# Optimization experiments

Hardware: AMD Instinct MI355X
Metric: run time of the kernel (lower is better)

Reference implementation:

```python
import jax, jax.numpy as jnp
import numpy as np

N, E, D, H, G = 50000, 800000, 256, 256, 64
EPS = 1e-5

def setup_inputs() -> dict:
    key = jax.random.key(0)
    ks = jax.random.split(key, 16)
    s_in = float(np.sqrt(2.0 / D))   # He fan_in init
    s_h = float(np.sqrt(2.0 / H))
    inp = {}
    inp['x'] = jax.random.normal(ks[0], (N, D), jnp.float32)
    inp['edge_index'] = jax.random.randint(ks[1], (2, E), 0, N)
    inp['batch'] = jnp.sort(jax.random.randint(ks[2], (N,), 0, G))
    inp['bn_in_g'] = jnp.ones((D,), jnp.float32)
    inp['bn_in_b'] = jnp.zeros((D,), jnp.float32)
    for i in range(3):
        fan = D if i == 0 else H
        inp[f'W{i}'] = jax.random.normal(ks[3 + i], (fan, H), jnp.float32) * float(np.sqrt(2.0 / fan))
        inp[f'b{i}'] = jnp.zeros((H,), jnp.float32)
        inp[f'bn{i}_g'] = jnp.ones((H,), jnp.float32)
        inp[f'bn{i}_b'] = jnp.zeros((H,), jnp.float32)
    inp['Wa1'] = jax.random.normal(ks[6], (H, H // 2), jnp.float32) * s_h
    inp['ba1'] = jnp.zeros((H // 2,), jnp.float32)
    inp['Wa2'] = jax.random.normal(ks[7], (H // 2, 1), jnp.float32) * float(np.sqrt(2.0 / (H // 2)))
    inp['ba2'] = jnp.zeros((1,), jnp.float32)
    inp['Wo'] = jax.random.normal(ks[8], (H, 2), jnp.float32) * s_h
    inp['bo'] = jnp.zeros((2,), jnp.float32)
    return inp


def _bn(x, g, b):
    # BatchNorm1d, batch statistics (training-mode normalization), biased var
    m = jnp.mean(x, axis=0)
    v = jnp.mean(jnp.square(x - m), axis=0)
    return (x - m) * jax.lax.rsqrt(v + EPS) * g + b


def _gcn(x, src, dst, W, b):
    h = x @ W  # [N, H]
    n = x.shape[0]
    deg = jax.ops.segment_sum(jnp.ones_like(src, x.dtype), dst, num_segments=n) + 1.0  # +1 self-loop
    dinv = jax.lax.rsqrt(deg)  # [N]
    msg = h[src] * (dinv[src] * dinv[dst])[:, None]          # gather + edgewise scale
    agg = jax.ops.segment_sum(msg, dst, num_segments=n)      # scatter-add at dst
    return agg + h * (dinv * dinv)[:, None] + b               # self-loop term fused


def reference(x, edge_index, batch, bn_in_g, bn_in_b,
              W0, b0, bn0_g, bn0_b, W1, b1, bn1_g, bn1_b, W2, b2, bn2_g, bn2_b,
              Wa1, ba1, Wa2, ba2, Wo, bo):
    src, dst = edge_index[0], edge_index[1]
    x = _bn(x, bn_in_g, bn_in_b)  # dropout = identity (eval)
    # layer 0
    xp = _bn(jax.nn.relu(_gcn(x, src, dst, W0, b0)), bn0_g, bn0_b)
    # layers 1..2 with residual
    for (W, b, g, bb) in ((W1, b1, bn1_g, bn1_b), (W2, b2, bn2_g, bn2_b)):
        xn = _bn(jax.nn.relu(_gcn(xp, src, dst, W, b)), g, bb)
        xp = xn + xp
    # attention over all nodes (softmax along node dim, as in source)
    scores = jax.nn.leaky_relu(xp @ Wa1 + ba1, 0.01) @ Wa2 + ba2  # [N,1]
    w = jax.nn.softmax(scores, axis=0)
    xw = xp * w
    cnt = jax.ops.segment_sum(jnp.ones((xp.shape[0],), xp.dtype), batch, num_segments=G)
    pooled = jax.ops.segment_sum(xw, batch, num_segments=G) / jnp.maximum(cnt, 1.0)[:, None]
    return pooled @ Wo + bo  # [G, 2]
```

## Files before the change

### kernel.cpp

```cpp
#include <hip/hip_runtime.h>

#define N_NODES 50000
#define N_EDGES 800000
#define DIM 256
#define NG 64
#define EPS_BN 1e-5f
#define NB_AGG 3125
#define NB_COL 512

typedef _Float16 f16;
typedef _Float16 half8 __attribute__((ext_vector_type(8)));
typedef _Float16 half4 __attribute__((ext_vector_type(4)));
typedef float floatx4 __attribute__((ext_vector_type(4)));

__global__ __launch_bounds__(256) void col_stats_kernel(const float* __restrict__ X, int n,
                                                        float* __restrict__ part) {
    int c = threadIdx.x;
    float s = 0.f, q = 0.f;
    for (int i = blockIdx.x; i < n; i += gridDim.x) {
        float v = X[(size_t)i * DIM + c];
        s += v; q += v * v;
    }
    part[(size_t)c * NB_COL + blockIdx.x] = s;
    part[(size_t)(DIM + c) * NB_COL + blockIdx.x] = q;
}

__global__ __launch_bounds__(256) void reduce_stats_kernel(const float* __restrict__ part, int nrows,
                                                           float* __restrict__ stats) {
    int wave = threadIdx.x >> 6, lane = threadIdx.x & 63;
    int c = blockIdx.x * 4 + wave;
    float t = 0.f;
    for (int i = lane; i < nrows; i += 64) t += part[(size_t)c * nrows + i];
    for (int o = 32; o > 0; o >>= 1) t += __shfl_down(t, o);
    if (lane == 0) stats[c] = t;
}

__global__ void finalize_stats_kernel(const float* __restrict__ sums, float* __restrict__ mr, float inv_n) {
    int c = threadIdx.x;
    float m = sums[c] * inv_n;
    float v = sums[DIM + c] * inv_n - m * m;
    mr[c] = m;
    mr[DIM + c] = rsqrtf(v + EPS_BN);
}

__global__ __launch_bounds__(256) void bn_apply_in_kernel(const float* __restrict__ Xin, f16* __restrict__ Af,
                                                          const float* __restrict__ mr, const float* __restrict__ g,
                                                          const float* __restrict__ b, int n) {
    int c = threadIdx.x;
    float mean = mr[c], rstd = mr[DIM + c], gg = g[c], bb = b[c];
    for (int i = blockIdx.x; i < n; i += gridDim.x) {
        size_t idx = (size_t)i * DIM + c;
        float v = Xin[idx];
        v = (v - mean) * rstd * gg + bb;
        Af[idx] = (f16)v;
    }
}

__global__ __launch_bounds__(256) void bn_apply_kernel(const f16* __restrict__ Cin, f16* __restrict__ Af,
                                                       const float* __restrict__ mr, const float* __restrict__ g,
                                                       const float* __restrict__ b, int n, int residual) {
    int c = threadIdx.x;
    float mean = mr[c], rstd = mr[DIM + c], gg = g[c], bb = b[c];
    for (int i = blockIdx.x; i < n; i += gridDim.x) {
        size_t idx = (size_t)i * DIM + c;
        float v = (float)Cin[idx];
        v = fmaxf(v, 0.f);
        v = (v - mean) * rstd * gg + bb;
        if (residual) v += (float)Af[idx];
        Af[idx] = (f16)v;
    }
}

__global__ void convert_wT_kernel(const float* __restrict__ W, f16* __restrict__ Wt, int K, int M) {
    int idx = blockIdx.x * 256 + threadIdx.x;
    if (idx < K * M) {
        int m = idx / K, k = idx % K;
        Wt[idx] = (f16)W[(size_t)k * M + m];
    }
}

__global__ void count_int_kernel(const int* __restrict__ idx, int n, int* __restrict__ cnt) {
    for (int i = blockIdx.x * blockDim.x + threadIdx.x; i < n; i += gridDim.x * blockDim.x)
        atomicAdd(&cnt[idx[i]], 1);
}

#define SCHUNK 2048
__global__ __launch_bounds__(256) void scan1_kernel(const int* __restrict__ cnt, int n,
                                                    int* __restrict__ outp, int* __restrict__ bsums,
                                                    float* __restrict__ dinv) {
    __shared__ int lds[256];
    int t = threadIdx.x;
    int base = blockIdx.x * SCHUNK + t * 8;
    int v[8]; int s = 0;
#pragma unroll
    for (int j = 0; j < 8; j++) {
        int id = base + j;
        int x = 0;
        if (id < n) { x = cnt[id]; dinv[id] = rsqrtf((float)x + 1.0f); }
        v[j] = s; s += x;
    }
    lds[t] = s; __syncthreads();
    for (int o = 1; o < 256; o <<= 1) {
        int add = (t >= o) ? lds[t - o] : 0;
        __syncthreads();
        lds[t] += add;
        __syncthreads();
    }
    int excl = lds[t] - s;
#pragma unroll
    for (int j = 0; j < 8; j++) { int id = base + j; if (id < n) outp[id] = excl + v[j]; }
    if (t == 255) bsums[blockIdx.x] = lds[255];
}

__global__ void scan2_kernel(int* bsums, int nb) {
    if (threadIdx.x == 0 && blockIdx.x == 0) {
        int r = 0;
        for (int i = 0; i < nb; i++) { int t = bsums[i]; bsums[i] = r; r += t; }
    }
}

__global__ void scan3_kernel(int* __restrict__ outp, const int* __restrict__ bsums, int n, int total) {
    int i = blockIdx.x * blockDim.x + threadIdx.x;
    if (i < n) outp[i] += bsums[i / SCHUNK];
    if (i == 0) outp[n] = total;
}

__global__ void scatter_kernel(const int* __restrict__ src, const int* __restrict__ dst, int ne,
                               const int* __restrict__ rowp, int* __restrict__ fill, int* __restrict__ ss) {
    for (int e = blockIdx.x * blockDim.x + threadIdx.x; e < ne; e += gridDim.x * blockDim.x) {
        int d = dst[e];
        int pos = rowp[d] + atomicAdd(&fill[d], 1);
        ss[pos] = src[e];
    }
}

__global__ void graph_bounds_kernel(const int* __restrict__ batch, int n, int* __restrict__ start) {
    int i = blockIdx.x * blockDim.x + threadIdx.x;
    if (i < n) {
        int b = batch[i];
        if (i == 0 || batch[i - 1] != b) start[b] = i;
    }
}

__global__ void graph_offsets2_kernel(const int* __restrict__ start, int* __restrict__ off, int* __restrict__ cnt) {
    if (threadIdx.x == 0 && blockIdx.x == 0) {
        int nxt = N_NODES;
        for (int g = NG - 1; g >= 0; --g) {
            int s = start[g];
            int o = (s < 0) ? nxt : s;
            off[g] = o;
            cnt[g] = nxt - o;
            nxt = o;
        }
    }
}

__global__ __launch_bounds__(256) void gcn_agg_kernel(const f16* __restrict__ h, const int* __restrict__ rowp,
                                                      const int* __restrict__ ss, const float* __restrict__ dinv,
                                                      const float* __restrict__ bias, f16* __restrict__ out,
                                                      float* __restrict__ part, int n) {
    int wave = threadIdx.x >> 6;
    int lane = threadIdx.x & 63;
    int c = lane * 4;
    float4 bv = *(const float4*)&bias[c];
    float s0 = 0.f, s1 = 0.f, s2 = 0.f, s3 = 0.f;
    float q0 = 0.f, q1 = 0.f, q2 = 0.f, q3 = 0.f;
    for (int row = blockIdx.x * 4 + wave; row < n; row += gridDim.x * 4) {
        float ax = 0.f, ay = 0.f, az = 0.f, aw = 0.f;
        int e0 = rowp[row], e1 = rowp[row + 1];
        int e = e0;
        for (; e + 3 < e1; e += 4) {
            int i0 = ss[e], i1 = ss[e + 1], i2 = ss[e + 2], i3 = ss[e + 3];
            float w0 = dinv[i0], w1 = dinv[i1], w2 = dinv[i2], w3 = dinv[i3];
            half4 h0 = *(const half4*)&h[(size_t)i0 * DIM + c];
            half4 h1 = *(const half4*)&h[(size_t)i1 * DIM + c];
            half4 h2 = *(const half4*)&h[(size_t)i2 * DIM + c];
            half4 h3 = *(const half4*)&h[(size_t)i3 * DIM + c];
            ax += w0 * (float)h0[0] + w1 * (float)h1[0] + w2 * (float)h2[0] + w3 * (float)h3[0];
            ay += w0 * (float)h0[1] + w1 * (float)h1[1] + w2 * (float)h2[1] + w3 * (float)h3[1];
            az += w0 * (float)h0[2] + w1 * (float)h1[2] + w2 * (float)h2[2] + w3 * (float)h3[2];
            aw += w0 * (float)h0[3] + w1 * (float)h1[3] + w2 * (float)h2[3] + w3 * (float)h3[3];
        }
        for (; e < e1; e++) {
            int si = ss[e];
            float ww = dinv[si];
            half4 hv = *(const half4*)&h[(size_t)si * DIM + c];
            ax += ww * (float)hv[0]; ay += ww * (float)hv[1];
            az += ww * (float)hv[2]; aw += ww * (float)hv[3];
        }
        float di = dinv[row];
        float d2 = di * di;
        half4 hs = *(const half4*)&h[(size_t)row * DIM + c];
        float rx = di * ax + d2 * (float)hs[0] + bv.x;
        float ry = di * ay + d2 * (float)hs[1] + bv.y;
        float rz = di * az + d2 * (float)hs[2] + bv.z;
        float rw = di * aw + d2 * (float)hs[3] + bv.w;
        half4 o; o[0] = (f16)rx; o[1] = (f16)ry; o[2] = (f16)rz; o[3] = (f16)rw;
        *(half4*)&out[(size_t)row * DIM + c] = o;
        float t;
        t = fmaxf(rx, 0.f); s0 += t; q0 += t * t;
        t = fmaxf(ry, 0.f); s1 += t; q1 += t * t;
        t = fmaxf(rz, 0.f); s2 += t; q2 += t * t;
        t = fmaxf(rw, 0.f); s3 += t; q3 += t * t;
    }
    __shared__ float sred[4][64][4];
    __shared__ float qred[4][64][4];
    sred[wave][lane][0] = s0; sred[wave][lane][1] = s1; sred[wave][lane][2] = s2; sred[wave][lane][3] = s3;
    qred[wave][lane][0] = q0; qred[wave][lane][1] = q1; qred[wave][lane][2] = q2; qred[wave][lane][3] = q3;
    __syncthreads();
    if (wave == 0) {
        int b = blockIdx.x;
#pragma unroll
        for (int j = 0; j < 4; j++) {
            float a = 0.f, qq = 0.f;
#pragma unroll
            for (int ww = 0; ww < 4; ww++) { a += sred[ww][lane][j]; qq += qred[ww][lane][j]; }
            part[(size_t)(c + j) * NB_AGG + b] = a;
            part[(size_t)(DIM + c + j) * NB_AGG + b] = qq;
        }
    }
}

#define BM 128
#define BN 128
#define BK 32
#define LDP 40
__global__ __launch_bounds__(256) void gemm_f16_kernel(const f16* __restrict__ Af, const f16* __restrict__ Wt,
                                                       f16* __restrict__ C, int n, int K, int M) {
    __shared__ __align__(16) f16 As[BM * LDP];
    __shared__ __align__(16) f16 Bs[BN * LDP];
    int tid = threadIdx.x;
    int wave = tid >> 6, lane = tid & 63;
    int wm = wave >> 1, wn = wave & 1;
    int q = lane >> 4, l16 = lane & 15;
    int bm = blockIdx.x * BM, bn = blockIdx.y * BN;
    floatx4 acc[4][4] = {};
    for (int k0 = 0; k0 < K; k0 += BK) {
#pragma unroll
        for (int rr = 0; rr < 2; rr++) {
            int cidx = tid + rr * 256;
            int row = cidx >> 2, off = (cidx & 3) * 8;
            int arow = bm + row; if (arow >= n) arow = n - 1;
            *(float4*)&As[row * LDP + off] = *(const float4*)&Af[(size_t)arow * K + k0 + off];
            int brow = bn + row;
            *(float4*)&Bs[row * LDP + off] = *(const float4*)&Wt[(size_t)brow * K + k0 + off];
        }
        __syncthreads();
        half8 af[4], bf[4];
#pragma unroll
        for (int i = 0; i < 4; i++) af[i] = *(half8*)&As[(wm * 64 + i * 16 + l16) * LDP + q * 8];
#pragma unroll
        for (int j = 0; j < 4; j++) bf[j] = *(half8*)&Bs[(wn * 64 + j * 16 + l16) * LDP + q * 8];
#pragma unroll
        for (int i = 0; i < 4; i++)
#pragma unroll
            for (int j = 0; j < 4; j++)
                acc[i][j] = __builtin_amdgcn_mfma_f32_16x16x32_f16(af[i], bf[j], acc[i][j], 0, 0, 0);
        __syncthreads();
    }
#pragma unroll
    for (int i = 0; i < 4; i++)
#pragma unroll
        for (int j = 0; j < 4; j++) {
            int col = bn + wn * 64 + j * 16 + l16;
#pragma unroll
            for (int r = 0; r < 4; r++) {
                int row = bm + wm * 64 + i * 16 + q * 4 + r;
                if (row < n) C[(size_t)row * M + col] = (f16)acc[i][j][r];
            }
        }
}

__global__ __launch_bounds__(256) void gemm_attn_kernel(const f16* __restrict__ Af, const f16* __restrict__ Wt,
                                                        const float* __restrict__ ba1, const float* __restrict__ Wa2,
                                                        const float* __restrict__ ba2, float* __restrict__ score,
                                                        int n, int K) {
    __shared__ __align__(16) f16 As[BM * LDP];
    __shared__ __align__(16) f16 Bs[128 * LDP];
    __shared__ float scred[128][2];
    int tid = threadIdx.x;
    int wave = tid >> 6, lane = tid & 63;
    int wm = wave >> 1, wn = wave & 1;
    int q = lane >> 4, l16 = lane & 15;
    int bm = blockIdx.x * BM;
    floatx4 acc[4][4] = {};
    for (int k0 = 0; k0 < K; k0 += BK) {
#pragma unroll
        for (int rr = 0; rr < 2; rr++) {
            int cidx = tid + rr * 256;
            int row = cidx >> 2, off = (cidx & 3) * 8;
            int arow = bm + row; if (arow >= n) arow = n - 1;
            *(float4*)&As[row * LDP + off] = *(const float4*)&Af[(size_t)arow * K + k0 + off];
            *(float4*)&Bs[row * LDP + off] = *(const float4*)&Wt[(size_t)row * K + k0 + off];
        }
        __syncthreads();
        half8 af[4], bf[4];
#pragma unroll
        for (int i = 0; i < 4; i++) af[i] = *(half8*)&As[(wm * 64 + i * 16 + l16) * LDP + q * 8];
#pragma unroll
        for (int j = 0; j < 4; j++) bf[j] = *(half8*)&Bs[(wn * 64 + j * 16 + l16) * LDP + q * 8];
#pragma unroll
        for (int i = 0; i < 4; i++)
#pragma unroll
            for (int j = 0; j < 4; j++)
                acc[i][j] = __builtin_amdgcn_mfma_f32_16x16x32_f16(af[i], bf[j], acc[i][j], 0, 0, 0);
        __syncthreads();
    }
    float ba1v[4], wa2v[4];
#pragma unroll
    for (int j = 0; j < 4; j++) {
        int col = wn * 64 + j * 16 + l16;
        ba1v[j] = ba1[col];
        wa2v[j] = Wa2[col];
    }
#pragma unroll
    for (int i = 0; i < 4; i++)
#pragma unroll
        for (int r = 0; r < 4; r++) {
            float p = 0.f;
#pragma unroll
            for (int j = 0; j < 4; j++) {
                float v = acc[i][j][r] + ba1v[j];
                v = (v > 0.f) ? v : 0.01f * v;
                p += v * wa2v[j];
            }
#pragma unroll
            for (int o = 1; o < 16; o <<= 1) p += __shfl_xor(p, o);
            if (l16 == 0) scred[wm * 64 + i * 16 + q * 4 + r][wn] = p;
        }
    __syncthreads();
    if (tid < 128) {
        int grow = bm + tid;
        if (grow < n) score[grow] = scred[tid][0] + scred[tid][1] + ba2[0];
    }
}

__global__ __launch_bounds__(256) void reduce_max_kernel(const float* __restrict__ s, int n, float* __restrict__ part) {
    __shared__ float lds[256];
    float m = -3.0e38f;
    for (int i = blockIdx.x * 256 + threadIdx.x; i < n; i += gridDim.x * 256) m = fmaxf(m, s[i]);
    lds[threadIdx.x] = m; __syncthreads();
    for (int o = 128; o > 0; o >>= 1) {
        if (threadIdx.x < o) lds[threadIdx.x] = fmaxf(lds[threadIdx.x], lds[threadIdx.x + o]);
        __syncthreads();
    }
    if (threadIdx.x == 0) part[blockIdx.x] = lds[0];
}

__global__ __launch_bounds__(256) void reduce_sumexp_kernel(const float* __restrict__ s, int n,
                                                            const float* __restrict__ part_max,
                                                            float* __restrict__ part_sum) {
    __shared__ float lds[256];
    int t = threadIdx.x;
    lds[t] = part_max[t]; __syncthreads();
    for (int o = 128; o > 0; o >>= 1) {
        if (t < o) lds[t] = fmaxf(lds[t], lds[t + o]);
        __syncthreads();
    }
    float mx = lds[0];
    __syncthreads();
    float acc = 0.f;
    for (int i = blockIdx.x * 256 + t; i < n; i += gridDim.x * 256) acc += expf(s[i] - mx);
    lds[t] = acc; __syncthreads();
    for (int o = 128; o > 0; o >>= 1) {
        if (t < o) lds[t] += lds[t + o];
        __syncthreads();
    }
    if (t == 0) part_sum[blockIdx.x] = lds[0];
}

__global__ __launch_bounds__(256) void pool_kernel(const f16* __restrict__ Af, const float* __restrict__ score,
                                                   const int* __restrict__ offs, const int* __restrict__ cnts,
                                                   const float* __restrict__ part_max, float* __restrict__ pooled) {
    __shared__ float lds[256];
    int c = threadIdx.x;
    lds[c] = part_max[c]; __syncthreads();
    for (int o = 128; o > 0; o >>= 1) {
        if (c < o) lds[c] = fmaxf(lds[c], lds[c + o]);
        __syncthreads();
    }
    float mx = lds[0];
    int g = blockIdx.x;
    int st = offs[g], cn = cnts[g];
    float acc = 0.f;
    for (int i = (int)blockIdx.y; i < cn; i += 32) {
        int i1 = i + 8, i2 = i + 16, i3 = i + 24;
        float s0 = score[st + i];
        float s1 = (i1 < cn) ? score[st + i1] : -3.0e38f;
        float s2 = (i2 < cn) ? score[st + i2] : -3.0e38f;
        float s3 = (i3 < cn) ? score[st + i3] : -3.0e38f;
        float a0 = (float)Af[(size_t)(st + i) * DIM + c];
        float a1 = (i1 < cn) ? (float)Af[(size_t)(st + i1) * DIM + c] : 0.f;
        float a2 = (i2 < cn) ? (float)Af[(size_t)(st + i2) * DIM + c] : 0.f;
        float a3 = (i3 < cn) ? (float)Af[(size_t)(st + i3) * DIM + c] : 0.f;
        acc += a0 * expf(s0 - mx) + a1 * expf(s1 - mx) + a2 * expf(s2 - mx) + a3 * expf(s3 - mx);
    }
    atomicAdd(&pooled[g * DIM + c], acc);
}

__global__ __launch_bounds__(256) void out_kernel(const float* __restrict__ pooled, const int* __restrict__ cnt,
                                                  const float* __restrict__ part_sum, const float* __restrict__ Wo,
                                                  const float* __restrict__ bo, float* __restrict__ out) {
    __shared__ float l0[256], l1[256];
    int g = blockIdx.x, c = threadIdx.x;
    l0[c] = part_sum[c]; __syncthreads();
    for (int o = 128; o > 0; o >>= 1) {
        if (c < o) l0[c] += l0[c + o];
        __syncthreads();
    }
    float denom = l0[0];
    __syncthreads();
    float scale = 1.f / (denom * fmaxf((float)cnt[g], 1.f));
    float v = pooled[g * DIM + c] * scale;
    l0[c] = v * Wo[c * 2];
    l1[c] = v * Wo[c * 2 + 1];
    __syncthreads();
    for (int o = 128; o > 0; o >>= 1) {
        if (c < o) { l0[c] += l0[c + o]; l1[c] += l1[c + o]; }
        __syncthreads();
    }
    if (c == 0) { out[g * 2] = l0[0] + bo[0]; out[g * 2 + 1] = l1[0] + bo[1]; }
}

extern "C" void kernel_launch(void* const* d_in, const int* in_sizes, int n_in,
                              void* d_out, int out_size, void* d_ws, size_t ws_size,
                              hipStream_t stream) {
    const float* x       = (const float*)d_in[0];
    const int*   ei      = (const int*)d_in[1];
    const int*   batch   = (const int*)d_in[2];
    const float* bn_in_g = (const float*)d_in[3];
    const float* bn_in_b = (const float*)d_in[4];
    const float* Ws[3]   = {(const float*)d_in[5],  (const float*)d_in[9],  (const float*)d_in[13]};
    const float* bs[3]   = {(const float*)d_in[6],  (const float*)d_in[10], (const float*)d_in[14]};
    const float* gs[3]   = {(const float*)d_in[7],  (const float*)d_in[11], (const float*)d_in[15]};
    const float* bbs[3]  = {(const float*)d_in[8],  (const float*)d_in[12], (const float*)d_in[16]};
    const float* Wa1 = (const float*)d_in[17];
    const float* ba1 = (const float*)d_in[18];
    const float* Wa2 = (const float*)d_in[19];
    const float* ba2 = (const float*)d_in[20];
    const float* Wo  = (const float*)d_in[21];
    const float* bo  = (const float*)d_in[22];

    char* w = (char*)d_ws;
    size_t off = 0;
    auto alloc = [&](size_t bytes) -> void* {
        void* p = w + off;
        off += (bytes + 255) & ~(size_t)255;
        return p;
    };
    int*   deg     = (int*)alloc((size_t)N_NODES * 4);
    int*   fill    = (int*)alloc((size_t)N_NODES * 4);
    float* pooled  = (float*)alloc((size_t)NG * DIM * 4);
    size_t zero_span = off;
    float* stats_part = (float*)alloc((size_t)512 * NB_AGG * 4);
    float* statsS  = (float*)alloc(512 * 4);
    f16*   Afh  = (f16*)alloc((size_t)N_NODES * DIM * 2);
    f16*   Bh   = (f16*)alloc((size_t)N_NODES * DIM * 2);
    f16*   Ch   = (f16*)alloc((size_t)N_NODES * DIM * 2);
    f16*   Wt[3];
    for (int l = 0; l < 3; l++) Wt[l] = (f16*)alloc((size_t)DIM * DIM * 2);
    f16*   Wa1t = (f16*)alloc((size_t)128 * DIM * 2);
    int* sorted_src = (int*)alloc((size_t)N_EDGES * 4);
    float* dinv = (float*)alloc((size_t)N_NODES * 4);
    int* rowp   = (int*)alloc((size_t)(N_NODES + 1) * 4);
    float* score = (float*)alloc((size_t)N_NODES * 4);
    float* mr    = (float*)alloc(512 * 4);
    int* bsums   = (int*)alloc(64 * 4);
    float* part_max = (float*)alloc(256 * 4);
    float* part_sum = (float*)alloc(256 * 4);
    int* gstart  = (int*)alloc(64 * 4);
    int* cnt_g   = (int*)alloc(64 * 4);
    int* off_g   = (int*)alloc(64 * 4);

    const int* src = ei;
    const int* dst = ei + N_EDGES;
    const int NSCAN = (N_NODES + SCHUNK - 1) / SCHUNK;

    hipMemsetAsync(d_ws, 0, zero_span, stream);
    hipMemsetAsync(gstart, 0xff, 64 * 4, stream);

    count_int_kernel<<<3125, 256, 0, stream>>>(dst, N_EDGES, deg);
    scan1_kernel<<<NSCAN, 256, 0, stream>>>(deg, N_NODES, rowp, bsums, dinv);
    scan2_kernel<<<1, 64, 0, stream>>>(bsums, NSCAN);
    scan3_kernel<<<(N_NODES + 255) / 256, 256, 0, stream>>>(rowp, bsums, N_NODES, N_EDGES);
    scatter_kernel<<<3125, 256, 0, stream>>>(src, dst, N_EDGES, rowp, fill, sorted_src);

    graph_bounds_kernel<<<(N_NODES + 255) / 256, 256, 0, stream>>>(batch, N_NODES, gstart);
    graph_offsets2_kernel<<<1, 64, 0, stream>>>(gstart, off_g, cnt_g);

    for (int l = 0; l < 3; l++)
        convert_wT_kernel<<<DIM * DIM / 256, 256, 0, stream>>>(Ws[l], Wt[l], DIM, DIM);
    convert_wT_kernel<<<128 * DIM / 256, 256, 0, stream>>>(Wa1, Wa1t, DIM, 128);

    col_stats_kernel<<<NB_COL, 256, 0, stream>>>(x, N_NODES, stats_part);
    reduce_stats_kernel<<<128, 256, 0, stream>>>(stats_part, NB_COL, statsS);
    finalize_stats_kernel<<<1, 256, 0, stream>>>(statsS, mr, 1.f / N_NODES);
    bn_apply_in_kernel<<<1024, 256, 0, stream>>>(x, Afh, mr, bn_in_g, bn_in_b, N_NODES);

    dim3 ggrid((N_NODES + BM - 1) / BM, DIM / BN);
    for (int l = 0; l < 3; l++) {
        gemm_f16_kernel<<<ggrid, 256, 0, stream>>>(Afh, Wt[l], Bh, N_NODES, DIM, DIM);
        gcn_agg_kernel<<<NB_AGG, 256, 0, stream>>>(Bh, rowp, sorted_src, dinv, bs[l], Ch, stats_part, N_NODES);
        reduce_stats_kernel<<<128, 256, 0, stream>>>(stats_part, NB_AGG, statsS);
        finalize_stats_kernel<<<1, 256, 0, stream>>>(statsS, mr, 1.f / N_NODES);
        bn_apply_kernel<<<1024, 256, 0, stream>>>(Ch, Afh, mr, gs[l], bbs[l], N_NODES, (l > 0) ? 1 : 0);
    }

    gemm_attn_kernel<<<(N_NODES + BM - 1) / BM, 256, 0, stream>>>(Afh, Wa1t, ba1, Wa2, ba2, score, N_NODES, DIM);
    reduce_max_kernel<<<256, 256, 0, stream>>>(score, N_NODES, part_max);
    reduce_sumexp_kernel<<<256, 256, 0, stream>>>(score, N_NODES, part_max, part_sum);

    pool_kernel<<<dim3(NG, 8), 256, 0, stream>>>(Afh, score, off_g, cnt_g, part_max, pooled);
    out_kernel<<<NG, 256, 0, stream>>>(pooled, cnt_g, part_sum, Wo, bo, (float*)d_out);
}
```

Before: 787.1 us.

## Fold source dinv scaling into GEMM epilogue and restructure BN stats reduction

The GEMM epilogue now multiplies each output row by dinv[row], so the aggregation kernel sums pre-scaled rows and applies only the destination dinv once. This removes the per-edge dinv gather and multiply from the gather loop. Separately, the per-block statistics partials are stored row-major, so the aggregation kernel writes them as coalesced float4 stores. The reduction becomes a two-stage split over NSPLIT chunks with coalesced column reads. Storing h already scaled by dinv in fp16 slightly changes rounding behaviour.

```diff
diff --git a/kernel.cpp b/kernel.cpp
--- a/kernel.cpp
+++ b/kernel.cpp
@@ -7,6 +7,7 @@
 #define EPS_BN 1e-5f
 #define NB_AGG 3125
 #define NB_COL 512
+#define NSPLIT 32
 
 typedef _Float16 f16;
 typedef _Float16 half8 __attribute__((ext_vector_type(8)));
@@ -21,24 +22,31 @@
         float v = X[(size_t)i * DIM + c];
         s += v; q += v * v;
     }
-    part[(size_t)c * NB_COL + blockIdx.x] = s;
-    part[(size_t)(DIM + c) * NB_COL + blockIdx.x] = q;
+    part[(size_t)blockIdx.x * 512 + c] = s;
+    part[(size_t)blockIdx.x * 512 + DIM + c] = q;
 }
 
 __global__ __launch_bounds__(256) void reduce_stats_kernel(const float* __restrict__ part, int nrows,
-                                                           float* __restrict__ stats) {
-    int wave = threadIdx.x >> 6, lane = threadIdx.x & 63;
-    int c = blockIdx.x * 4 + wave;
+                                                           float* __restrict__ p2) {
+    int col = blockIdx.x * 256 + threadIdx.x;
+    int chunk = (nrows + NSPLIT - 1) / NSPLIT;
+    int r0 = blockIdx.y * chunk;
+    int r1 = min(r0 + chunk, nrows);
     float t = 0.f;
-    for (int i = lane; i < nrows; i += 64) t += part[(size_t)c * nrows + i];
-    for (int o = 32; o > 0; o >>= 1) t += __shfl_down(t, o);
-    if (lane == 0) stats[c] = t;
-}
-
-__global__ void finalize_stats_kernel(const float* __restrict__ sums, float* __restrict__ mr, float inv_n) {
+    for (int r = r0; r < r1; r++) t += part[(size_t)r * 512 + col];
+    p2[(size_t)blockIdx.y * 512 + col] = t;
+}
+
+__global__ void finalize_stats_kernel(const float* __restrict__ p2, float* __restrict__ mr, float inv_n) {
     int c = threadIdx.x;
-    float m = sums[c] * inv_n;
-    float v = sums[DIM + c] * inv_n - m * m;
+    float s = 0.f, q = 0.f;
+#pragma unroll
+    for (int r = 0; r < NSPLIT; r++) {
+        s += p2[(size_t)r * 512 + c];
+        q += p2[(size_t)r * 512 + DIM + c];
+    }
+    float m = s * inv_n;
+    float v = q * inv_n - m * m;
     mr[c] = m;
     mr[DIM + c] = rsqrtf(v + EPS_BN);
 }
@@ -171,30 +179,26 @@
         int e = e0;
         for (; e + 3 < e1; e += 4) {
             int i0 = ss[e], i1 = ss[e + 1], i2 = ss[e + 2], i3 = ss[e + 3];
-            float w0 = dinv[i0], w1 = dinv[i1], w2 = dinv[i2], w3 = dinv[i3];
             half4 h0 = *(const half4*)&h[(size_t)i0 * DIM + c];
             half4 h1 = *(const half4*)&h[(size_t)i1 * DIM + c];
             half4 h2 = *(const half4*)&h[(size_t)i2 * DIM + c];
             half4 h3 = *(const half4*)&h[(size_t)i3 * DIM + c];
-            ax += w0 * (float)h0[0] + w1 * (float)h1[0] + w2 * (float)h2[0] + w3 * (float)h3[0];
-            ay += w0 * (float)h0[1] + w1 * (float)h1[1] + w2 * (float)h2[1] + w3 * (float)h3[1];
-            az += w0 * (float)h0[2] + w1 * (float)h1[2] + w2 * (float)h2[2] + w3 * (float)h3[2];
-            aw += w0 * (float)h0[3] + w1 * (float)h1[3] + w2 * (float)h2[3] + w3 * (float)h3[3];
+            ax += (float)h0[0] + (float)h1[0] + (float)h2[0] + (float)h3[0];
+            ay += (float)h0[1] + (float)h1[1] + (float)h2[1] + (float)h3[1];
+            az += (float)h0[2] + (float)h1[2] + (float)h2[2] + (float)h3[2];
+            aw += (float)h0[3] + (float)h1[3] + (float)h2[3] + (float)h3[3];
         }
         for (; e < e1; e++) {
             int si = ss[e];
-            float ww = dinv[si];
             half4 hv = *(const half4*)&h[(size_t)si * DIM + c];
-            ax += ww * (float)hv[0]; ay += ww * (float)hv[1];
-            az += ww * (float)hv[2]; aw += ww * (float)hv[3];
+            ax += (float)hv[0]; ay += (float)hv[1]; az += (float)hv[2]; aw += (float)hv[3];
         }
         float di = dinv[row];
-        float d2 = di * di;
         half4 hs = *(const half4*)&h[(size_t)row * DIM + c];
-        float rx = di * ax + d2 * (float)hs[0] + bv.x;
-        float ry = di * ay + d2 * (float)hs[1] + bv.y;
-        float rz = di * az + d2 * (float)hs[2] + bv.z;
-        float rw = di * aw + d2 * (float)hs[3] + bv.w;
+        float rx = di * (ax + (float)hs[0]) + bv.x;
+        float ry = di * (ay + (float)hs[1]) + bv.y;
+        float rz = di * (az + (float)hs[2]) + bv.z;
+        float rw = di * (aw + (float)hs[3]) + bv.w;
         half4 o; o[0] = (f16)rx; o[1] = (f16)ry; o[2] = (f16)rz; o[3] = (f16)rw;
         *(half4*)&out[(size_t)row * DIM + c] = o;
         float t;
@@ -209,15 +213,15 @@
     qred[wave][lane][0] = q0; qred[wave][lane][1] = q1; qred[wave][lane][2] = q2; qred[wave][lane][3] = q3;
     __syncthreads();
     if (wave == 0) {
-        int b = blockIdx.x;
-#pragma unroll
-        for (int j = 0; j < 4; j++) {
-            float a = 0.f, qq = 0.f;
-#pragma unroll
-            for (int ww = 0; ww < 4; ww++) { a += sred[ww][lane][j]; qq += qred[ww][lane][j]; }
-            part[(size_t)(c + j) * NB_AGG + b] = a;
-            part[(size_t)(DIM + c + j) * NB_AGG + b] = qq;
-        }
+        size_t base = (size_t)blockIdx.x * 512;
+        float4 a = make_float4(0.f, 0.f, 0.f, 0.f), qv = make_float4(0.f, 0.f, 0.f, 0.f);
+#pragma unroll
+        for (int ww = 0; ww < 4; ww++) {
+            a.x += sred[ww][lane][0]; a.y += sred[ww][lane][1]; a.z += sred[ww][lane][2]; a.w += sred[ww][lane][3];
+            qv.x += qred[ww][lane][0]; qv.y += qred[ww][lane][1]; qv.z += qred[ww][lane][2]; qv.w += qred[ww][lane][3];
+        }
+        *(float4*)&part[base + c] = a;
+        *(float4*)&part[base + DIM + c] = qv;
     }
 }
 
@@ -226,7 +230,8 @@
 #define BK 32
 #define LDP 40
 __global__ __launch_bounds__(256) void gemm_f16_kernel(const f16* __restrict__ Af, const f16* __restrict__ Wt,
-                                                       f16* __restrict__ C, int n, int K, int M) {
+                                                       f16* __restrict__ C, const float* __restrict__ scale,
+                                                       int n, int K, int M) {
     __shared__ __align__(16) f16 As[BM * LDP];
     __shared__ __align__(16) f16 Bs[BN * LDP];
     int tid = threadIdx.x;
@@ -259,16 +264,20 @@
         __syncthreads();
     }
 #pragma unroll
-    for (int i = 0; i < 4; i++)
-#pragma unroll
-        for (int j = 0; j < 4; j++) {
-            int col = bn + wn * 64 + j * 16 + l16;
-#pragma unroll
-            for (int r = 0; r < 4; r++) {
-                int row = bm + wm * 64 + i * 16 + q * 4 + r;
-                if (row < n) C[(size_t)row * M + col] = (f16)acc[i][j][r];
+    for (int i = 0; i < 4; i++) {
+#pragma unroll
+        for (int r = 0; r < 4; r++) {
+            int row = bm + wm * 64 + i * 16 + q * 4 + r;
+            if (row < n) {
+                float sc = scale ? scale[row] : 1.0f;
+#pragma unroll
+                for (int j = 0; j < 4; j++) {
+                    int col = bn + wn * 64 + j * 16 + l16;
+                    C[(size_t)row * M + col] = (f16)(acc[i][j][r] * sc);
+                }
             }
         }
+    }
 }
 
 __global__ __launch_bounds__(256) void gemm_attn_kernel(const f16* __restrict__ Af, const f16* __restrict__ Wt,
@@ -452,8 +461,8 @@
     int*   fill    = (int*)alloc((size_t)N_NODES * 4);
     float* pooled  = (float*)alloc((size_t)NG * DIM * 4);
     size_t zero_span = off;
-    float* stats_part = (float*)alloc((size_t)512 * NB_AGG * 4);
-    float* statsS  = (float*)alloc(512 * 4);
+    float* stats_part = (float*)alloc((size_t)NB_AGG * 512 * 4);
+    float* stats_p2   = (float*)alloc((size_t)NSPLIT * 512 * 4);
     f16*   Afh  = (f16*)alloc((size_t)N_NODES * DIM * 2);
     f16*   Bh   = (f16*)alloc((size_t)N_NODES * DIM * 2);
     f16*   Ch   = (f16*)alloc((size_t)N_NODES * DIM * 2);
@@ -493,16 +502,16 @@
     convert_wT_kernel<<<128 * DIM / 256, 256, 0, stream>>>(Wa1, Wa1t, DIM, 128);
 
     col_stats_kernel<<<NB_COL, 256, 0, stream>>>(x, N_NODES, stats_part);
-    reduce_stats_kernel<<<128, 256, 0, stream>>>(stats_part, NB_COL, statsS);
-    finalize_stats_kernel<<<1, 256, 0, stream>>>(statsS, mr, 1.f / N_NODES);
+    reduce_stats_kernel<<<dim3(2, NSPLIT), 256, 0, stream>>>(stats_part, NB_COL, stats_p2);
+    finalize_stats_kernel<<<1, 256, 0, stream>>>(stats_p2, mr, 1.f / N_NODES);
     bn_apply_in_kernel<<<1024, 256, 0, stream>>>(x, Afh, mr, bn_in_g, bn_in_b, N_NODES);
 
     dim3 ggrid((N_NODES + BM - 1) / BM, DIM / BN);
     for (int l = 0; l < 3; l++) {
-        gemm_f16_kernel<<<ggrid, 256, 0, stream>>>(Afh, Wt[l], Bh, N_NODES, DIM, DIM);
+        gemm_f16_kernel<<<ggrid, 256, 0, stream>>>(Afh, Wt[l], Bh, dinv, N_NODES, DIM, DIM);
         gcn_agg_kernel<<<NB_AGG, 256, 0, stream>>>(Bh, rowp, sorted_src, dinv, bs[l], Ch, stats_part, N_NODES);
-        reduce_stats_kernel<<<128, 256, 0, stream>>>(stats_part, NB_AGG, statsS);
-        finalize_stats_kernel<<<1, 256, 0, stream>>>(statsS, mr, 1.f / N_NODES);
+        reduce_stats_kernel<<<dim3(2, NSPLIT), 256, 0, stream>>>(stats_part, NB_AGG, stats_p2);
+        finalize_stats_kernel<<<1, 256, 0, stream>>>(stats_p2, mr, 1.f / N_NODES);
         bn_apply_kernel<<<1024, 256, 0, stream>>>(Ch, Afh, mr, gs[l], bbs[l], N_NODES, (l > 0) ? 1 : 0);
     }
 
```

Result: faster. 765.0 us (-2.8%).
